# Kernel optimization log

Hardware: AMD Instinct MI355X
Metric: run time of the kernel (lower is better)

The kernel has to match this reference:

```python
import jax, jax.numpy as jnp
import numpy as np

N_HEAD = 16

def setup_inputs() -> dict:
    key = jax.random.key(0)
    ks = jax.random.split(key, 5)
    C = 1024
    s = 1.0 / np.sqrt(C)
    x = jax.random.normal(ks[0], (2, 2048, C), dtype=jnp.float32)
    wq = jax.random.normal(ks[1], (C, C), dtype=jnp.float32) * s
    wk = jax.random.normal(ks[2], (C, C), dtype=jnp.float32) * s
    wv = jax.random.normal(ks[3], (C, C), dtype=jnp.float32) * s
    wp = jax.random.normal(ks[4], (C, C), dtype=jnp.float32) * s
    z = jnp.zeros((C,), dtype=jnp.float32)
    return {"x": x, "wq": wq, "bq": z, "wk": wk, "bk": z,
            "wv": wv, "bv": z, "wp": wp, "bp": z}

def reference(x, wq, bq, wk, bk, wv, bv, wp, bp):
    B, T, C = x.shape
    H = N_HEAD
    D = C // H
    # projections: weights stored as (in, out) -> x @ w + b
    q = (x @ wq + bq).reshape(B, T, H, D).transpose(0, 2, 1, 3)  # [B,H,T,D]
    k = (x @ wk + bk).reshape(B, T, H, D).transpose(0, 2, 1, 3)
    v = (x @ wv + bv).reshape(B, T, H, D).transpose(0, 2, 1, 3)
    att = jnp.einsum('bhqd,bhkd->bhqk', q, k) / jnp.sqrt(jnp.float32(D))
    causal = jnp.tril(jnp.ones((T, T), dtype=bool))
    att = jnp.where(causal[None, None], att, -jnp.inf)
    att = jax.nn.softmax(att, axis=-1)
    out = jnp.einsum('bhqk,bhkd->bhqd', att, v)  # [B,H,T,D]
    out = out.transpose(0, 2, 1, 3).reshape(B, T, C)
    return out @ wp + bp
```

## Files before the change

### kernel.cpp

```cpp
#include <hip/hip_runtime.h>
#include <hip/hip_bf16.h>
#include <stdint.h>


typedef __attribute__((ext_vector_type(8))) short bf16x8;
typedef __attribute__((ext_vector_type(4))) float f32x4;
typedef __attribute__((ext_vector_type(4))) short short4v;

#define MFMA16(a,b,c) __builtin_amdgcn_mfma_f32_16x16x32_bf16(a,b,c,0,0,0)

__device__ __forceinline__ unsigned short f2bfu(float f){
  union { __hip_bfloat16 h; unsigned short u; } cv;
  cv.h = __float2bfloat16(f);
  return cv.u;
}

__device__ __forceinline__ unsigned cvtpk(float a, float b){
  unsigned r;
  asm("v_cvt_pk_bf16_f32 %0, %1, %2" : "=v"(r) : "v"(a), "v"(b));
  return r;
}

__device__ __forceinline__ void async16(const void* g, void* s){
  __builtin_amdgcn_global_load_lds((const __attribute__((address_space(1))) void*)g,
                                   (__attribute__((address_space(3))) void*)s, 16, 0, 0);
}

__global__ __launch_bounds__(256)
void prep_k(const float* __restrict__ x, unsigned short* __restrict__ xb,
            const float* __restrict__ wq, const float* __restrict__ wk,
            const float* __restrict__ wv, const float* __restrict__ wp,
            unsigned short* __restrict__ wqkvT, unsigned short* __restrict__ wpT)
{
  __shared__ float t[32][33];
  const int bx = blockIdx.x;
  const int tid = threadIdx.x;
  if (bx < 4096) {
    const int i = bx * 256 + tid;
    const float4 v = ((const float4*)x)[i];
    short4v o;
    o.x = (short)f2bfu(v.x); o.y = (short)f2bfu(v.y);
    o.z = (short)f2bfu(v.z); o.w = (short)f2bfu(v.w);
    ((short4v*)xb)[i] = o;
    return;
  }
  const int b = bx - 4096;
  const int wsel = b >> 10;
  const float* W = (wsel == 0) ? wq : (wsel == 1) ? wk : (wsel == 2) ? wv : wp;
  unsigned short* Wt = (wsel == 3) ? wpT : wqkvT + (size_t)wsel * 1024 * 1024;
  const int bc = ((b & 1023) & 31) * 32;
  const int br = ((b & 1023) >> 5) * 32;
  const int tx = tid & 31, ty = tid >> 5;
  #pragma unroll
  for (int i = 0; i < 32; i += 8)
    t[ty + i][tx] = W[(size_t)(br + ty + i) * 1024 + bc + tx];
  __syncthreads();
  #pragma unroll
  for (int i = 0; i < 32; i += 8)
    Wt[(size_t)(bc + ty + i) * 1024 + br + tx] = f2bfu(t[tx][ty + i]);
}

__global__ __launch_bounds__(256) void transpose_v_k(const unsigned short* __restrict__ V,
                                                     unsigned short* __restrict__ VT){
  __shared__ unsigned short tile[64][72];
  const int bh = blockIdx.y;
  const int t0 = blockIdx.x * 64;
  const int tid = threadIdx.x;
  const int r = tid >> 2;
  const int c = (tid & 3) * 16;
  const unsigned short* src = V + ((size_t)bh * 2048 + t0 + r) * 64 + c;
  *(uint4*)&tile[r][c]     = *(const uint4*)(src);
  *(uint4*)&tile[r][c + 8] = *(const uint4*)(src + 8);
  __syncthreads();
  const int d = tid >> 2;
  const int tt = (tid & 3) * 16;
  alignas(16) unsigned short tmp[16];
  #pragma unroll
  for (int j = 0; j < 16; j++) tmp[j] = tile[tt + j][d];
  unsigned short* dst = VT + ((size_t)bh * 64 + d) * 2048 + t0 + tt;
  *(uint4*)dst       = *(uint4*)&tmp[0];
  *(uint4*)(dst + 8) = *(uint4*)&tmp[8];
}

template<int MODE>
__global__ __launch_bounds__(256)
void gemm_bt(const unsigned short* __restrict__ A, const unsigned short* __restrict__ Bt,
             const float* __restrict__ b0, const float* __restrict__ b1, const float* __restrict__ b2,
             unsigned short* __restrict__ Qo, unsigned short* __restrict__ Ko,
             unsigned short* __restrict__ Vo, float* __restrict__ Fo, int N)
{
  constexpr int K = 1024;
  __shared__ unsigned short As[128 * 32];
  __shared__ unsigned short Bs[128 * 32];
  const int tid = threadIdx.x;
  const int lane = tid & 63;
  const int w = tid >> 6;
  const int l15 = lane & 15, lhi = lane >> 4;
  const int row0 = blockIdx.y * 128;
  const int col0 = blockIdx.x * 128;
  const int wr = (w >> 1) * 64;
  const int wc = (w & 1) * 64;

  f32x4 acc[4][4];
  #pragma unroll
  for (int i = 0; i < 4; i++)
    #pragma unroll
    for (int j = 0; j < 4; j++) acc[i][j] = 0.0f;

  const int srow = lane >> 2;
  const int scol = (lane & 3) * 8;
  const unsigned short* Ab = A  + (size_t)(row0 + w * 32 + srow) * K + scol;
  const unsigned short* Bb = Bt + (size_t)(col0 + w * 32 + srow) * K + scol;
  unsigned short* AsW = As + (w * 32) * 32;
  unsigned short* BsW = Bs + (w * 32) * 32;

  for (int k0 = 0; k0 < K; k0 += 32) {
    __syncthreads();
    async16(Ab + k0,          AsW);
    async16(Ab + k0 + 16 * K, AsW + 16 * 32);
    async16(Bb + k0,          BsW);
    async16(Bb + k0 + 16 * K, BsW + 16 * 32);
    __syncthreads();
    bf16x8 af[4], bfv[4];
    #pragma unroll
    for (int i = 0; i < 4; i++) {
      af[i]  = *(const bf16x8*)&As[(wr + i * 16 + l15) * 32 + lhi * 8];
      bfv[i] = *(const bf16x8*)&Bs[(wc + i * 16 + l15) * 32 + lhi * 8];
    }
    #pragma unroll
    for (int i = 0; i < 4; i++)
      #pragma unroll
      for (int j = 0; j < 4; j++)
        acc[i][j] = MFMA16(af[i], bfv[j], acc[i][j]);
  }

  #pragma unroll
  for (int j = 0; j < 4; j++) {
    const int n = col0 + wc + j * 16 + l15;
    if constexpr (MODE == 0) {
      const int which = n >> 10;
      const int cn = n & 1023;
      const float bias = (which == 0 ? b0[cn] : which == 1 ? b1[cn] : b2[cn]);
      unsigned short* dst = (which == 0 ? Qo : which == 1 ? Ko : Vo);
      const float sc = (which == 0 ? 0.125f * 1.44269504f : 1.0f);
      const int h = cn >> 6, d = cn & 63;
      #pragma unroll
      for (int i = 0; i < 4; i++)
        #pragma unroll
        for (int r = 0; r < 4; r++) {
          const int m = row0 + wr + i * 16 + lhi * 4 + r;
          const int b_ = m >> 11, t = m & 2047;
          dst[(((size_t)(b_ * 16 + h) * 2048 + t) * 64) + d] =
              f2bfu((acc[i][j][r] + bias) * sc);
        }
    } else {
      const float bias = b0[n];
      #pragma unroll
      for (int i = 0; i < 4; i++)
        #pragma unroll
        for (int r = 0; r < 4; r++) {
          const int m = row0 + wr + i * 16 + lhi * 4 + r;
          Fo[(size_t)m * N + n] = acc[i][j][r] + bias;
        }
    }
  }
}


__device__ __forceinline__ void attn_tile(
    const unsigned short* __restrict__ Ksb, const unsigned short* __restrict__ Vsb,
    unsigned short* __restrict__ Pw,
    bf16x8 q0f, bf16x8 q1f, f32x4 (&o)[4],
    float& mrun, float& lrun,
    int l15, int lhi, int q0, int kv0, bool mask)
{
  f32x4 s[4];
  __builtin_amdgcn_s_setprio(1);
  #pragma unroll
  for (int nf = 0; nf < 4; ++nf) {
    const int rk = nf * 16 + l15;
    const int swz = (rk & 7) << 4;
    const bf16x8 kf0 = *(const bf16x8*)((const char*)Ksb + ((rk * 128 + lhi * 16) ^ swz));
    const bf16x8 kf1 = *(const bf16x8*)((const char*)Ksb + ((rk * 128 + 64 + lhi * 16) ^ swz));
    s[nf] = 0.0f;
    s[nf] = MFMA16(kf0, q0f, s[nf]);
    s[nf] = MFMA16(kf1, q1f, s[nf]);
  }
  __builtin_amdgcn_s_setprio(0);

  if (mask) {
    const int q = q0 + l15;
    #pragma unroll
    for (int nf = 0; nf < 4; ++nf)
      #pragma unroll
      for (int r = 0; r < 4; r++) {
        const int kv = kv0 + nf * 16 + lhi * 4 + r;
        if (kv > q) s[nf][r] = -1e30f;
      }
  }

  float m0 = fmaxf(fmaxf(s[0][0], s[0][1]), fmaxf(s[0][2], s[0][3]));
  float m1 = fmaxf(fmaxf(s[1][0], s[1][1]), fmaxf(s[1][2], s[1][3]));
  float m2 = fmaxf(fmaxf(s[2][0], s[2][1]), fmaxf(s[2][2], s[2][3]));
  float m3 = fmaxf(fmaxf(s[3][0], s[3][1]), fmaxf(s[3][2], s[3][3]));
  float pm = fmaxf(fmaxf(m0, m1), fmaxf(m2, m3));
  pm = fmaxf(pm, __shfl_xor(pm, 16, 64));
  pm = fmaxf(pm, __shfl_xor(pm, 32, 64));

  if (__any((int)(pm > mrun + 8.0f))) {
    const float mnew = fmaxf(mrun, pm);
    const float sc = exp2f(mrun - mnew);
    mrun = mnew;
    lrun *= sc;
    float scr[4];
    #pragma unroll
    for (int r = 0; r < 4; r++) scr[r] = __shfl(sc, lhi * 4 + r, 64);
    #pragma unroll
    for (int nf = 0; nf < 4; nf++)
      #pragma unroll
      for (int r = 0; r < 4; r++) o[nf][r] *= scr[r];
  }

  float rs = 0.0f;
  const int swz = (l15 & 7) << 4;
  #pragma unroll
  for (int nf = 0; nf < 4; nf++) {
    float p0 = exp2f(s[nf][0] - mrun);
    float p1 = exp2f(s[nf][1] - mrun);
    float p2 = exp2f(s[nf][2] - mrun);
    float p3 = exp2f(s[nf][3] - mrun);
    rs += (p0 + p1) + (p2 + p3);
    uint2 pk;
    pk.x = cvtpk(p0, p1);
    pk.y = cvtpk(p2, p3);
    *(uint2*)((char*)Pw + ((l15 * 128 + nf * 32 + lhi * 8) ^ swz)) = pk;
  }
  rs += __shfl_xor(rs, 16, 64);
  rs += __shfl_xor(rs, 32, 64);
  lrun += rs;

  const bf16x8 pf0 = *(const bf16x8*)((const char*)Pw + ((l15 * 128 + lhi * 16) ^ swz));
  const bf16x8 pf1 = *(const bf16x8*)((const char*)Pw + ((l15 * 128 + 64 + lhi * 16) ^ swz));

  __builtin_amdgcn_s_setprio(1);
  #pragma unroll
  for (int nf = 0; nf < 4; nf++) {
    const int rv = nf * 16 + l15;
    const int swv = (rv & 7) << 4;
    const bf16x8 vf0 = *(const bf16x8*)((const char*)Vsb + ((rv * 128 + lhi * 16) ^ swv));
    const bf16x8 vf1 = *(const bf16x8*)((const char*)Vsb + ((rv * 128 + 64 + lhi * 16) ^ swv));
    o[nf] = MFMA16(pf0, vf0, o[nf]);
    o[nf] = MFMA16(pf1, vf1, o[nf]);
  }
  __builtin_amdgcn_s_setprio(0);
}

__global__ __launch_bounds__(256)
void attn_k(const unsigned short* __restrict__ Q, const unsigned short* __restrict__ Kg,
            const unsigned short* __restrict__ VT, unsigned short* __restrict__ O)
{
  __shared__ unsigned short Ks[2][64 * 64];
  __shared__ unsigned short Vs[2][64 * 64];
  __shared__ alignas(16) unsigned short Ps[4][1024];
  const int bh = blockIdx.y, bx = blockIdx.x;
  const int b_ = bh >> 4, h = bh & 15;
  const int tid = threadIdx.x, lane = tid & 63, w = tid >> 6;
  const int l15 = lane & 15, lhi = lane >> 4;
  const int tA = bx * 4 + w, tB = 127 - tA;
  const int q0A = tA * 16, q0B = tB * 16;
  const int jmA = bx, jmB = 31 - bx;

  const unsigned short* Kbh  = Kg + (size_t)bh * (2048 * 64);
  const unsigned short* VTbh = VT + (size_t)bh * (64 * 2048);
  unsigned short* Pw = &Ps[w][0];

  const unsigned short* QpA = Q + ((size_t)bh * 2048 + q0A + l15) * 64 + lhi * 8;
  const unsigned short* QpB = Q + ((size_t)bh * 2048 + q0B + l15) * 64 + lhi * 8;
  const bf16x8 qfA0 = *(const bf16x8*)(QpA);
  const bf16x8 qfA1 = *(const bf16x8*)(QpA + 32);
  const bf16x8 qfB0 = *(const bf16x8*)(QpB);
  const bf16x8 qfB1 = *(const bf16x8*)(QpB + 32);

  f32x4 oA[4], oB[4];
  #pragma unroll
  for (int nf = 0; nf < 4; nf++) { oA[nf] = 0.0f; oB[nf] = 0.0f; }
  float mA = -1e30f, lA = 0.0f, mB = -1e30f, lB = 0.0f;

  const int srow = w * 8 + (lane >> 3);
  const int cole = (((lane & 7) ^ (lane >> 3)) << 3);
  const unsigned short* Ksrc = Kbh + (size_t)srow * 64 + cole;
  const unsigned short* Vsrc = VTbh + (size_t)srow * 2048 + cole;

  auto stage = [&](int kv0, int buf) {
    unsigned short* kb = &Ks[buf][w * 512];
    unsigned short* vb = &Vs[buf][w * 512];
    #pragma unroll
    for (int it = 0; it < 2; ++it) {
      async16(Ksrc + (size_t)(kv0 + it * 32) * 64, kb + it * 2048);
      async16(Vsrc + (size_t)(it * 32) * 2048 + kv0, vb + it * 2048);
    }
  };

  stage(0, 0);
  __syncthreads();

  int cur = 0;
  for (int j = 0; j <= jmB; ++j) {
    if (j < jmB) stage((j + 1) * 64, cur ^ 1);
    const int kv0 = j * 64;
    attn_tile(&Ks[cur][0], &Vs[cur][0], Pw, qfB0, qfB1,
              oB, mB, lB, l15, lhi, q0B, kv0, j == jmB);
    if (j <= jmA)
      attn_tile(&Ks[cur][0], &Vs[cur][0], Pw, qfA0, qfA1,
                oA, mA, lA, l15, lhi, q0A, kv0, j == jmA);
    __syncthreads();
    cur ^= 1;
  }

  const float linvA = 1.0f / lA, linvB = 1.0f / lB;
  float invA[4], invB[4];
  #pragma unroll
  for (int r = 0; r < 4; r++) {
    invA[r] = __shfl(linvA, lhi * 4 + r, 64);
    invB[r] = __shfl(linvB, lhi * 4 + r, 64);
  }
  #pragma unroll
  for (int nf = 0; nf < 4; nf++)
    #pragma unroll
    for (int r = 0; r < 4; r++) {
      const int c = h * 64 + nf * 16 + l15;
      O[((size_t)b_ * 2048 + q0A + lhi * 4 + r) * 1024 + c] = f2bfu(oA[nf][r] * invA[r]);
      O[((size_t)b_ * 2048 + q0B + lhi * 4 + r) * 1024 + c] = f2bfu(oB[nf][r] * invB[r]);
    }
}


extern "C" void kernel_launch(void* const* d_in, const int* in_sizes, int n_in,
                              void* d_out, int out_size, void* d_ws, size_t ws_size,
                              hipStream_t stream) {
  const float* x  = (const float*)d_in[0];
  const float* wq = (const float*)d_in[1];
  const float* bq = (const float*)d_in[2];
  const float* wk = (const float*)d_in[3];
  const float* bk = (const float*)d_in[4];
  const float* wv = (const float*)d_in[5];
  const float* bv = (const float*)d_in[6];
  const float* wp = (const float*)d_in[7];
  const float* bp = (const float*)d_in[8];
  float* out = (float*)d_out;

  char* ws = (char*)d_ws;
  const size_t MB = 1024 * 1024;
  unsigned short* xb    = (unsigned short*)(ws);
  unsigned short* wqkvT = (unsigned short*)(ws + 8  * MB);
  unsigned short* wpT   = (unsigned short*)(ws + 14 * MB);
  unsigned short* Qb    = (unsigned short*)(ws + 16 * MB);
  unsigned short* Kb    = (unsigned short*)(ws + 24 * MB);
  unsigned short* Vb    = (unsigned short*)(ws + 32 * MB);
  unsigned short* VTb   = (unsigned short*)(ws);
  unsigned short* Ob    = (unsigned short*)(ws + 32 * MB);

  prep_k<<<dim3(8192), dim3(256), 0, stream>>>(x, xb, wq, wk, wv, wp, wqkvT, wpT);

  gemm_bt<0><<<dim3(24, 32), dim3(256), 0, stream>>>(xb, wqkvT, bq, bk, bv,
                                                     Qb, Kb, Vb, nullptr, 3072);
  transpose_v_k<<<dim3(32, 32), dim3(256), 0, stream>>>(Vb, VTb);
  attn_k<<<dim3(16, 32), dim3(256), 0, stream>>>(Qb, Kb, VTb, Ob);
  gemm_bt<1><<<dim3(8, 32), dim3(256), 0, stream>>>(Ob, wpT, bp, nullptr, nullptr,
                                                    nullptr, nullptr, nullptr, out, 1024);
}
```

Measured before the change: 134.1 us.

## Fuse V transpose into QKV GEMM epilogue and interleave attention tiles

The QKV GEMM epilogue now writes V directly in transposed [bh][d][t] layout with packed bf16 stores, so the separate transpose kernel and its launch go away. The attention loop is restructured so the two query tiles (A and B) share the K and V fragment loads from LDS and interleave their MFMAs, with a separate P buffer per tile. Blocks are also remapped so that neighbouring block IDs cover different heads, which changes how the causal workload spreads across CUs. The cost is higher register pressure from holding both score tiles and more LDS for the doubled P buffer.

```diff
diff --git a/kernel.cpp b/kernel.cpp
--- a/kernel.cpp
+++ b/kernel.cpp
@@ -58,28 +58,6 @@
   #pragma unroll
   for (int i = 0; i < 32; i += 8)
     Wt[(size_t)(bc + ty + i) * 1024 + br + tx] = f2bfu(t[tx][ty + i]);
-}
-
-__global__ __launch_bounds__(256) void transpose_v_k(const unsigned short* __restrict__ V,
-                                                     unsigned short* __restrict__ VT){
-  __shared__ unsigned short tile[64][72];
-  const int bh = blockIdx.y;
-  const int t0 = blockIdx.x * 64;
-  const int tid = threadIdx.x;
-  const int r = tid >> 2;
-  const int c = (tid & 3) * 16;
-  const unsigned short* src = V + ((size_t)bh * 2048 + t0 + r) * 64 + c;
-  *(uint4*)&tile[r][c]     = *(const uint4*)(src);
-  *(uint4*)&tile[r][c + 8] = *(const uint4*)(src + 8);
-  __syncthreads();
-  const int d = tid >> 2;
-  const int tt = (tid & 3) * 16;
-  alignas(16) unsigned short tmp[16];
-  #pragma unroll
-  for (int j = 0; j < 16; j++) tmp[j] = tile[tt + j][d];
-  unsigned short* dst = VT + ((size_t)bh * 64 + d) * 2048 + t0 + tt;
-  *(uint4*)dst       = *(uint4*)&tmp[0];
-  *(uint4*)(dst + 8) = *(uint4*)&tmp[8];
 }
 
 template<int MODE>
@@ -141,18 +119,30 @@
       const int which = n >> 10;
       const int cn = n & 1023;
       const float bias = (which == 0 ? b0[cn] : which == 1 ? b1[cn] : b2[cn]);
-      unsigned short* dst = (which == 0 ? Qo : which == 1 ? Ko : Vo);
-      const float sc = (which == 0 ? 0.125f * 1.44269504f : 1.0f);
       const int h = cn >> 6, d = cn & 63;
-      #pragma unroll
-      for (int i = 0; i < 4; i++)
+      if (which == 2) {
         #pragma unroll
-        for (int r = 0; r < 4; r++) {
-          const int m = row0 + wr + i * 16 + lhi * 4 + r;
+        for (int i = 0; i < 4; i++) {
+          const int m = row0 + wr + i * 16 + lhi * 4;
           const int b_ = m >> 11, t = m & 2047;
-          dst[(((size_t)(b_ * 16 + h) * 2048 + t) * 64) + d] =
-              f2bfu((acc[i][j][r] + bias) * sc);
+          uint2 pk;
+          pk.x = cvtpk(acc[i][j][0] + bias, acc[i][j][1] + bias);
+          pk.y = cvtpk(acc[i][j][2] + bias, acc[i][j][3] + bias);
+          *(uint2*)(Vo + (((size_t)(b_ * 16 + h) * 64 + d) * 2048 + t)) = pk;
         }
+      } else {
+        unsigned short* dst = (which == 0 ? Qo : Ko);
+        const float sc = (which == 0 ? 0.125f * 1.44269504f : 1.0f);
+        #pragma unroll
+        for (int i = 0; i < 4; i++)
+          #pragma unroll
+          for (int r = 0; r < 4; r++) {
+            const int m = row0 + wr + i * 16 + lhi * 4 + r;
+            const int b_ = m >> 11, t = m & 2047;
+            dst[(((size_t)(b_ * 16 + h) * 2048 + t) * 64) + d] =
+                f2bfu((acc[i][j][r] + bias) * sc);
+          }
+      }
     } else {
       const float bias = b0[n];
       #pragma unroll
@@ -167,27 +157,10 @@
 }
 
 
-__device__ __forceinline__ void attn_tile(
-    const unsigned short* __restrict__ Ksb, const unsigned short* __restrict__ Vsb,
-    unsigned short* __restrict__ Pw,
-    bf16x8 q0f, bf16x8 q1f, f32x4 (&o)[4],
-    float& mrun, float& lrun,
-    int l15, int lhi, int q0, int kv0, bool mask)
+__device__ __forceinline__ void softmax_pack(
+    f32x4 (&s)[4], f32x4 (&o)[4], float& mrun, float& lrun,
+    unsigned short* __restrict__ Pw, int l15, int lhi, int q0, int kv0, bool mask)
 {
-  f32x4 s[4];
-  __builtin_amdgcn_s_setprio(1);
-  #pragma unroll
-  for (int nf = 0; nf < 4; ++nf) {
-    const int rk = nf * 16 + l15;
-    const int swz = (rk & 7) << 4;
-    const bf16x8 kf0 = *(const bf16x8*)((const char*)Ksb + ((rk * 128 + lhi * 16) ^ swz));
-    const bf16x8 kf1 = *(const bf16x8*)((const char*)Ksb + ((rk * 128 + 64 + lhi * 16) ^ swz));
-    s[nf] = 0.0f;
-    s[nf] = MFMA16(kf0, q0f, s[nf]);
-    s[nf] = MFMA16(kf1, q1f, s[nf]);
-  }
-  __builtin_amdgcn_s_setprio(0);
-
   if (mask) {
     const int q = q0 + l15;
     #pragma unroll
@@ -198,7 +171,6 @@
         if (kv > q) s[nf][r] = -1e30f;
       }
   }
-
   float m0 = fmaxf(fmaxf(s[0][0], s[0][1]), fmaxf(s[0][2], s[0][3]));
   float m1 = fmaxf(fmaxf(s[1][0], s[1][1]), fmaxf(s[1][2], s[1][3]));
   float m2 = fmaxf(fmaxf(s[2][0], s[2][1]), fmaxf(s[2][2], s[2][3]));
@@ -238,21 +210,6 @@
   rs += __shfl_xor(rs, 16, 64);
   rs += __shfl_xor(rs, 32, 64);
   lrun += rs;
-
-  const bf16x8 pf0 = *(const bf16x8*)((const char*)Pw + ((l15 * 128 + lhi * 16) ^ swz));
-  const bf16x8 pf1 = *(const bf16x8*)((const char*)Pw + ((l15 * 128 + 64 + lhi * 16) ^ swz));
-
-  __builtin_amdgcn_s_setprio(1);
-  #pragma unroll
-  for (int nf = 0; nf < 4; nf++) {
-    const int rv = nf * 16 + l15;
-    const int swv = (rv & 7) << 4;
-    const bf16x8 vf0 = *(const bf16x8*)((const char*)Vsb + ((rv * 128 + lhi * 16) ^ swv));
-    const bf16x8 vf1 = *(const bf16x8*)((const char*)Vsb + ((rv * 128 + 64 + lhi * 16) ^ swv));
-    o[nf] = MFMA16(pf0, vf0, o[nf]);
-    o[nf] = MFMA16(pf1, vf1, o[nf]);
-  }
-  __builtin_amdgcn_s_setprio(0);
 }
 
 __global__ __launch_bounds__(256)
@@ -261,8 +218,10 @@
 {
   __shared__ unsigned short Ks[2][64 * 64];
   __shared__ unsigned short Vs[2][64 * 64];
-  __shared__ alignas(16) unsigned short Ps[4][1024];
-  const int bh = blockIdx.y, bx = blockIdx.x;
+  __shared__ alignas(16) unsigned short Ps[4][2048];
+  const int flat = blockIdx.y * 16 + blockIdx.x;
+  const int u = (flat & 7) * 64 + (flat >> 3);
+  const int bx = u & 15, bh = u >> 4;
   const int b_ = bh >> 4, h = bh & 15;
   const int tid = threadIdx.x, lane = tid & 63, w = tid >> 6;
   const int l15 = lane & 15, lhi = lane >> 4;
@@ -272,7 +231,8 @@
 
   const unsigned short* Kbh  = Kg + (size_t)bh * (2048 * 64);
   const unsigned short* VTbh = VT + (size_t)bh * (64 * 2048);
-  unsigned short* Pw = &Ps[w][0];
+  unsigned short* PwB = &Ps[w][0];
+  unsigned short* PwA = &Ps[w][1024];
 
   const unsigned short* QpA = Q + ((size_t)bh * 2048 + q0A + l15) * 64 + lhi * 8;
   const unsigned short* QpB = Q + ((size_t)bh * 2048 + q0B + l15) * 64 + lhi * 8;
@@ -308,11 +268,57 @@
   for (int j = 0; j <= jmB; ++j) {
     if (j < jmB) stage((j + 1) * 64, cur ^ 1);
     const int kv0 = j * 64;
-    attn_tile(&Ks[cur][0], &Vs[cur][0], Pw, qfB0, qfB1,
-              oB, mB, lB, l15, lhi, q0B, kv0, j == jmB);
-    if (j <= jmA)
-      attn_tile(&Ks[cur][0], &Vs[cur][0], Pw, qfA0, qfA1,
-                oA, mA, lA, l15, lhi, q0A, kv0, j == jmA);
+    const bool doA = (j <= jmA);
+    const unsigned short* Ksb = &Ks[cur][0];
+    const unsigned short* Vsb = &Vs[cur][0];
+
+    f32x4 sB[4], sA[4];
+    __builtin_amdgcn_s_setprio(1);
+    #pragma unroll
+    for (int nf = 0; nf < 4; ++nf) {
+      const int rk = nf * 16 + l15;
+      const int swzk = (rk & 7) << 4;
+      const bf16x8 kf0 = *(const bf16x8*)((const char*)Ksb + ((rk * 128 + lhi * 16) ^ swzk));
+      const bf16x8 kf1 = *(const bf16x8*)((const char*)Ksb + ((rk * 128 + 64 + lhi * 16) ^ swzk));
+      sB[nf] = 0.0f;
+      sB[nf] = MFMA16(kf0, qfB0, sB[nf]);
+      sB[nf] = MFMA16(kf1, qfB1, sB[nf]);
+      if (doA) {
+        sA[nf] = 0.0f;
+        sA[nf] = MFMA16(kf0, qfA0, sA[nf]);
+        sA[nf] = MFMA16(kf1, qfA1, sA[nf]);
+      }
+    }
+    __builtin_amdgcn_s_setprio(0);
+
+    softmax_pack(sB, oB, mB, lB, PwB, l15, lhi, q0B, kv0, j == jmB);
+    if (doA) softmax_pack(sA, oA, mA, lA, PwA, l15, lhi, q0A, kv0, j == jmA);
+
+    const int swzp = (l15 & 7) << 4;
+    const bf16x8 pfB0 = *(const bf16x8*)((const char*)PwB + ((l15 * 128 + lhi * 16) ^ swzp));
+    const bf16x8 pfB1 = *(const bf16x8*)((const char*)PwB + ((l15 * 128 + 64 + lhi * 16) ^ swzp));
+    bf16x8 pfA0, pfA1;
+    if (doA) {
+      pfA0 = *(const bf16x8*)((const char*)PwA + ((l15 * 128 + lhi * 16) ^ swzp));
+      pfA1 = *(const bf16x8*)((const char*)PwA + ((l15 * 128 + 64 + lhi * 16) ^ swzp));
+    }
+
+    __builtin_amdgcn_s_setprio(1);
+    #pragma unroll
+    for (int nf = 0; nf < 4; nf++) {
+      const int rv = nf * 16 + l15;
+      const int swzv = (rv & 7) << 4;
+      const bf16x8 vf0 = *(const bf16x8*)((const char*)Vsb + ((rv * 128 + lhi * 16) ^ swzv));
+      const bf16x8 vf1 = *(const bf16x8*)((const char*)Vsb + ((rv * 128 + 64 + lhi * 16) ^ swzv));
+      oB[nf] = MFMA16(pfB0, vf0, oB[nf]);
+      oB[nf] = MFMA16(pfB1, vf1, oB[nf]);
+      if (doA) {
+        oA[nf] = MFMA16(pfA0, vf0, oA[nf]);
+        oA[nf] = MFMA16(pfA1, vf1, oA[nf]);
+      }
+    }
+    __builtin_amdgcn_s_setprio(0);
+
     __syncthreads();
     cur ^= 1;
   }
@@ -356,15 +362,13 @@
   unsigned short* wpT   = (unsigned short*)(ws + 14 * MB);
   unsigned short* Qb    = (unsigned short*)(ws + 16 * MB);
   unsigned short* Kb    = (unsigned short*)(ws + 24 * MB);
-  unsigned short* Vb    = (unsigned short*)(ws + 32 * MB);
-  unsigned short* VTb   = (unsigned short*)(ws);
-  unsigned short* Ob    = (unsigned short*)(ws + 32 * MB);
+  unsigned short* VTb   = (unsigned short*)(ws + 32 * MB);
+  unsigned short* Ob    = (unsigned short*)(ws);
 
   prep_k<<<dim3(8192), dim3(256), 0, stream>>>(x, xb, wq, wk, wv, wp, wqkvT, wpT);
 
   gemm_bt<0><<<dim3(24, 32), dim3(256), 0, stream>>>(xb, wqkvT, bq, bk, bv,
-                                                     Qb, Kb, Vb, nullptr, 3072);
-  transpose_v_k<<<dim3(32, 32), dim3(256), 0, stream>>>(Vb, VTb);
+                                                     Qb, Kb, VTb, nullptr, 3072);
   attn_k<<<dim3(16, 32), dim3(256), 0, stream>>>(Qb, Kb, VTb, Ob);
   gemm_bt<1><<<dim3(8, 32), dim3(256), 0, stream>>>(Ob, wpT, bp, nullptr, nullptr,
                                                     nullptr, nullptr, nullptr, out, 1024);
```

Measured after the change: 128.8 us. 3.9% less time.
